# Optimization experiments

Hardware: AMD Instinct MI355X
Metric: run time of the kernel (lower is better)

The kernel has to match this reference:

```python
import jax, jax.numpy as jnp
import numpy as np

N_LAYERS = 4
EPS = 1e-5  # eqx.nn.LayerNorm default


def _kernels(lam, P, B, C, step, L):
    # Annotated-S4 DPLR generating-function kernel (Q = P), vectorized over H channels.
    # lam, P, B, C: (H, N) complex64; step: (H, 1) real. Returns K: (H, L) real.
    omega = jnp.exp((-2j * jnp.pi) * (jnp.arange(L) / L))            # (L,) roots of unity
    g = (2.0 / step) * ((1.0 - omega) / (1.0 + omega))[None, :]      # (H, L) bilinear warp
    c = 2.0 / (1.0 + omega)                                          # (L,)

    def cauchy(v):  # v: (H, N) -> (H, L): sum_n v_n / (g - lambda_n)
        return jnp.sum(v[:, None, :] / (g[:, :, None] - lam[:, None, :]), axis=-1)

    k00 = cauchy(jnp.conj(C) * B)
    k01 = cauchy(jnp.conj(C) * P)
    k10 = cauchy(jnp.conj(P) * B)
    k11 = cauchy(jnp.conj(P) * P)
    at_roots = c[None, :] * (k00 - k01 * (1.0 / (1.0 + k11)) * k10)  # woodbury correction
    return jnp.fft.ifft(at_roots, n=L, axis=-1).real                 # (H, L)


def _causal_conv(u, K):
    # u: (B, L, H) real input, K: (H, L) real kernel -> causal conv along L via zero-padded FFT.
    L = u.shape[1]
    Ud = jnp.fft.rfft(u, n=2 * L, axis=1)                 # (B, F, H)
    Kd = jnp.fft.rfft(K, n=2 * L, axis=-1)                # (H, F)
    return jnp.fft.irfft(Ud * Kd.T[None], n=2 * L, axis=1)[:, :L]


def _forward(x, enc_w, enc_b, dec_w, dec_b, lam_re, lam_im, p_re, p_im, b_re, b_im,
             c_re, c_im, d, log_step, norm_w, norm_b, w1, b1, w2, b2):
    L = x.shape[1]
    h = x @ enc_w.T + enc_b                               # encoder: (B, L, H)
    for i in range(N_LAYERS):
        skip = h
        mu = h.mean(-1, keepdims=True)
        var = ((h - mu) ** 2).mean(-1, keepdims=True)
        hn = (h - mu) / jnp.sqrt(var + EPS) * norm_w[i] + norm_b[i]
        K = _kernels(lam_re[i] + 1j * lam_im[i], p_re[i] + 1j * p_im[i],
                     b_re[i] + 1j * b_im[i], c_re[i] + 1j * c_im[i],
                     jnp.exp(log_step[i])[:, None], L)
        y = _causal_conv(hn, K) + hn * d[i]               # SSM conv + skip-through D term
        y = jax.nn.gelu(y)
        y = (y @ w1[i].T + b1[i]) * jax.nn.sigmoid(y @ w2[i].T + b2[i])  # gated MLP
        h = skip + y
    return h @ dec_w.T + dec_b                            # decoder: (B, L, out)


def setup_inputs() -> dict:
    key = jax.random.key(0)
    B, L, IN, OUT, H, N, NL = 8, 2048, 64, 64, 128, 64, N_LAYERS
    ks = jax.random.split(key, 12)
    rn = lambda k, s, sc: (jax.random.normal(k, s) * sc).astype(jnp.float32)
    return dict(
        x=rn(ks[0], (B, L, IN), 1.0),
        convolve=1,
        enc_w=rn(ks[1], (H, IN), 1.0 / np.sqrt(IN)), enc_b=jnp.zeros((H,), jnp.float32),
        dec_w=rn(ks[2], (OUT, H), 1.0 / np.sqrt(H)), dec_b=jnp.zeros((OUT,), jnp.float32),
        lam_re=-0.5 * jnp.ones((NL, H, N), jnp.float32),  # HiPPO/S4D-style stable poles
        lam_im=jnp.tile(jnp.float32(np.pi) * jnp.arange(N, dtype=jnp.float32), (NL, H, 1)),
        p_re=rn(ks[3], (NL, H, N), 0.5 / np.sqrt(N)), p_im=rn(ks[4], (NL, H, N), 0.5 / np.sqrt(N)),
        b_re=rn(ks[5], (NL, H, N), 1.0), b_im=rn(ks[6], (NL, H, N), 1.0),
        c_re=rn(ks[7], (NL, H, N), 1.0 / np.sqrt(N)), c_im=rn(ks[8], (NL, H, N), 1.0 / np.sqrt(N)),
        d=jnp.ones((NL, H), jnp.float32),
        log_step=(jax.random.uniform(ks[9], (NL, H)) * (np.log(0.1) - np.log(0.001))
                  + np.log(0.001)).astype(jnp.float32),
        norm_w=jnp.ones((NL, H), jnp.float32), norm_b=jnp.zeros((NL, H), jnp.float32),
        w1=rn(ks[10], (NL, H, H), 1.0 / np.sqrt(H)), b1=jnp.zeros((NL, H), jnp.float32),
        w2=rn(ks[11], (NL, H, H), 1.0 / np.sqrt(H)), b2=jnp.zeros((NL, H), jnp.float32),
    )


def reference(x, convolve, enc_w, enc_b, dec_w, dec_b, lam_re, lam_im, p_re, p_im,
              b_re, b_im, c_re, c_im, d, log_step, norm_w, norm_b, w1, b1, w2, b2):
    # convolve is static 1 (True): the FFT-convolution path of the S4 Model.
    return _forward(x, enc_w, enc_b, dec_w, dec_b, lam_re, lam_im, p_re, p_im, b_re, b_im,
                    c_re, c_im, d, log_step, norm_w, norm_b, w1, b1, w2, b2)
```

## Files before the change

kernel.cpp:

```cpp
#include <hip/hip_runtime.h>
#include <hip/hip_bf16.h>


#define Bsz 8
#define Lseq 2048
#define Hdim 128
#define Npol 64
#define NLAYERS 4

typedef __bf16 bf16x8 __attribute__((ext_vector_type(8)));
typedef float f32x16 __attribute__((ext_vector_type(16)));

__device__ __forceinline__ float fast_rcp(float x) { return __builtin_amdgcn_rcpf(x); }
__device__ __forceinline__ float fast_rsq(float x) { return __builtin_amdgcn_rsqf(x); }

__device__ __forceinline__ float2 cmulf(float2 a, float2 b) {
    return make_float2(a.x * b.x - a.y * b.y, a.x * b.y + a.y * b.x);
}
__device__ __forceinline__ float2 cmulc(float2 a, float2 b) {
    return make_float2(a.x * b.x + a.y * b.y, a.y * b.x - a.x * b.y);
}

__device__ __forceinline__ float gelu_f(float v) {
    float z = 0.7978845608028654f * (v + 0.044715f * v * v * v);
    float e = __expf(2.0f * z);
    return v - v * fast_rcp(e + 1.0f);
}

__device__ __forceinline__ int sw(int i) { return (i & ~15) | ((i ^ (i >> 4)) & 15); }

static __device__ const float W16R[8] = {1.f, 0.9238795325f, 0.7071067812f, 0.3826834324f,
                                         0.f, -0.3826834324f, -0.7071067812f, -0.9238795325f};
static __device__ const float W16I[8] = {0.f, -0.3826834324f, -0.7071067812f, -0.9238795325f,
                                         -1.f, -0.9238795325f, -0.7071067812f, -0.3826834324f};
static __device__ const int BR4[16] = {0, 8, 4, 12, 2, 10, 6, 14, 1, 9, 5, 13, 3, 11, 7, 15};
static __device__ const int BR3[8] = {0, 4, 2, 6, 1, 5, 3, 7};

__device__ __forceinline__ float2 twget(const float2* __restrict__ tw, int e) {
    float2 w = tw[e & 2047];
    if (e & 2048) { w.x = -w.x; w.y = -w.y; }
    return w;
}

template <bool INV>
__device__ __forceinline__ void fft16_dif(float2 v[16]) {
#pragma unroll
    for (int mi = 0; mi < 4; mi++) {
        const int m = 8 >> mi;
#pragma unroll
        for (int g = 0; g < 16; g += 2 * m) {
#pragma unroll
            for (int j = 0; j < m; j++) {
                float wr = W16R[j << mi];
                float wi = INV ? -W16I[j << mi] : W16I[j << mi];
                float2 a = v[g + j], b = v[g + j + m];
                float dx = a.x - b.x, dy = a.y - b.y;
                v[g + j] = make_float2(a.x + b.x, a.y + b.y);
                v[g + j + m] = make_float2(dx * wr - dy * wi, dx * wi + dy * wr);
            }
        }
    }
}

template <bool INV>
__device__ __forceinline__ void fft16_dit(float2 v[16]) {
#pragma unroll
    for (int mi = 3; mi >= 0; mi--) {
        const int m = 8 >> mi;
#pragma unroll
        for (int g = 0; g < 16; g += 2 * m) {
#pragma unroll
            for (int j = 0; j < m; j++) {
                float wr = W16R[j << mi];
                float wi = INV ? -W16I[j << mi] : W16I[j << mi];
                float2 a = v[g + j], b = v[g + j + m];
                float bx = b.x * wr - b.y * wi, by = b.x * wi + b.y * wr;
                v[g + j] = make_float2(a.x + bx, a.y + by);
                v[g + j + m] = make_float2(a.x - bx, a.y - by);
            }
        }
    }
}

template <bool INV>
__device__ __forceinline__ void fft8_dif(float2 v[8]) {
#pragma unroll
    for (int mi = 0; mi < 3; mi++) {
        const int m = 4 >> mi;
#pragma unroll
        for (int g = 0; g < 8; g += 2 * m) {
#pragma unroll
            for (int j = 0; j < m; j++) {
                float wr = W16R[j << (mi + 1)];
                float wi = INV ? -W16I[j << (mi + 1)] : W16I[j << (mi + 1)];
                float2 a = v[g + j], b = v[g + j + m];
                float dx = a.x - b.x, dy = a.y - b.y;
                v[g + j] = make_float2(a.x + b.x, a.y + b.y);
                v[g + j + m] = make_float2(dx * wr - dy * wi, dx * wi + dy * wr);
            }
        }
    }
}

__device__ __forceinline__ void fft4096_passA_hz(float2* data, const float2* __restrict__ tw,
                                                 int t, const float2 vin[8]) {
    float2 v[16];
#pragma unroll
    for (int j = 0; j < 8; j++) v[j] = vin[j];
#pragma unroll
    for (int j = 0; j < 8; j++)
        v[j + 8] = cmulf(v[j], make_float2(W16R[j], W16I[j]));
#pragma unroll
    for (int mi = 1; mi < 4; mi++) {
        const int m = 8 >> mi;
#pragma unroll
        for (int g = 0; g < 16; g += 2 * m) {
#pragma unroll
            for (int j = 0; j < m; j++) {
                float wr = W16R[j << mi], wi = W16I[j << mi];
                float2 a = v[g + j], b = v[g + j + m];
                float dx = a.x - b.x, dy = a.y - b.y;
                v[g + j] = make_float2(a.x + b.x, a.y + b.y);
                v[g + j + m] = make_float2(dx * wr - dy * wi, dx * wi + dy * wr);
            }
        }
    }
#pragma unroll
    for (int i = 1; i < 16; i++) v[i] = cmulf(v[i], twget(tw, t * BR4[i]));
#pragma unroll
    for (int i = 0; i < 16; i++) data[sw(i * 256 + t)] = v[i];
}

__device__ __forceinline__ void fft4096_fwd_BC(float2* data, const float2* __restrict__ tw, int t) {
    __syncthreads();
    {
        int j0 = t & 15;
        int base = (t >> 4) * 256 + j0;
        float2 v[16];
#pragma unroll
        for (int k = 0; k < 16; k++) v[k] = data[sw(base + 16 * k)];
        fft16_dif<false>(v);
#pragma unroll
        for (int i = 1; i < 16; i++) v[i] = cmulf(v[i], twget(tw, 16 * j0 * BR4[i]));
#pragma unroll
        for (int i = 0; i < 16; i++) data[sw(base + 16 * i)] = v[i];
    }
    __syncthreads();
    {
        float2 v[16];
#pragma unroll
        for (int k = 0; k < 16; k++) v[k] = data[sw(t * 16 + k)];
        fft16_dif<false>(v);
#pragma unroll
        for (int i = 0; i < 16; i++) data[sw(t * 16 + i)] = v[i];
    }
    __syncthreads();
}

__device__ __forceinline__ void kfft_core(int hh, int t, float* smem,
                                          float2* __restrict__ KdL,
                                          const float2* __restrict__ tw,
                                          const float* __restrict__ lam_re,
                                          const float* __restrict__ lam_im,
                                          const float* __restrict__ p_re,
                                          const float* __restrict__ p_im,
                                          const float* __restrict__ b_re,
                                          const float* __restrict__ b_im,
                                          const float* __restrict__ c_re,
                                          const float* __restrict__ c_im,
                                          const float* __restrict__ log_step) {
    float2* data = (float2*)smem;
    float* ktmp = smem + 8192;
    float4* polA = (float4*)(smem + 10240);
    float4* polB = (float4*)(smem + 10496);
    float* n11S = smem + 10752;
    int baseP = hh * Npol;
    if (t < Npol) {
        int n = t;
        float lr = lam_re[baseP + n], li = lam_im[baseP + n];
        float pr = p_re[baseP + n], pi = p_im[baseP + n];
        float br = b_re[baseP + n], bi = b_im[baseP + n];
        float cr = c_re[baseP + n], ci = c_im[baseP + n];
        polA[n] = make_float4(lr, li, cr * br + ci * bi, cr * bi - ci * br);
        polB[n] = make_float4(cr * pr + ci * pi, cr * pi - ci * pr,
                              pr * br + pi * bi, pr * bi - pi * br);
        n11S[n] = pr * pr + pi * pi;
    }
    __syncthreads();
    {
        float step = expf(log_step[hh]);
        float gs = 2.0f / step;
        float wrv[8], wiv[8];
        float gr[8], gi[8];
#pragma unroll
        for (int j = 0; j < 8; j++) {
            int l = t + 256 * j;
            float ang = -6.283185307179586f * (float)l / (float)Lseq;
            float wr = cosf(ang), wi = sinf(ang);
            wrv[j] = wr; wiv[j] = wi;
            float dr = 1.0f + wr, di = wi;
            float invd2 = fast_rcp(dr * dr + di * di);
            float nr = 1.0f - wr, ni = -wi;
            gr[j] = gs * (nr * dr + ni * di) * invd2;
            gi[j] = gs * (ni * dr - nr * di) * invd2;
        }
        float k00x[8], k00y[8], k01x[8], k01y[8];
        float k10x[8], k10y[8], k11x[8], k11y[8];
#pragma unroll
        for (int j = 0; j < 8; j++) {
            k00x[j] = 0.f; k00y[j] = 0.f; k01x[j] = 0.f; k01y[j] = 0.f;
            k10x[j] = 0.f; k10y[j] = 0.f; k11x[j] = 0.f; k11y[j] = 0.f;
        }
        for (int n = 0; n < Npol; n++) {
            float4 A = polA[n];
            float4 B = polB[n];
            float n11 = n11S[n];
#pragma unroll
            for (int j = 0; j < 8; j++) {
                float er = gr[j] - A.x, ei = gi[j] - A.y;
                float inv2 = fast_rcp(fmaf(er, er, ei * ei));
                float ir = er * inv2;
                float mi = ei * inv2;
                k00x[j] = fmaf(A.z, ir, fmaf(A.w, mi, k00x[j]));
                k00y[j] = fmaf(A.w, ir, fmaf(-A.z, mi, k00y[j]));
                k01x[j] = fmaf(B.x, ir, fmaf(B.y, mi, k01x[j]));
                k01y[j] = fmaf(B.y, ir, fmaf(-B.x, mi, k01y[j]));
                k10x[j] = fmaf(B.z, ir, fmaf(B.w, mi, k10x[j]));
                k10y[j] = fmaf(B.w, ir, fmaf(-B.z, mi, k10y[j]));
                k11x[j] = fmaf(n11, ir, k11x[j]);
                k11y[j] = fmaf(-n11, mi, k11y[j]);
            }
        }
#pragma unroll
        for (int j = 0; j < 8; j++) {
            int l = t + 256 * j;
            float dr = 1.0f + wrv[j], di = wiv[j];
            float invd2 = fast_rcp(dr * dr + di * di);
            float cr2 = 2.0f * dr * invd2, ci2 = -2.0f * di * invd2;
            float wr2 = 1.0f + k11x[j], wi2 = k11y[j];
            float w2inv = fast_rcp(fmaf(wr2, wr2, wi2 * wi2));
            float vr = wr2 * w2inv, vi = -wi2 * w2inv;
            float t1x = k01x[j] * k10x[j] - k01y[j] * k10y[j];
            float t1y = k01x[j] * k10y[j] + k01y[j] * k10x[j];
            float t2x = t1x * vr - t1y * vi, t2y = t1x * vi + t1y * vr;
            float ex = k00x[j] - t2x, ey = k00y[j] - t2y;
            data[sw(l)] = make_float2(cr2 * ex - ci2 * ey, cr2 * ey + ci2 * ex);
        }
    }
    __syncthreads();
    if (t < 128) {
        float2 v[16];
#pragma unroll
        for (int k = 0; k < 16; k++) v[k] = data[sw(t + 128 * k)];
        fft16_dif<true>(v);
#pragma unroll
        for (int i = 1; i < 16; i++) v[i] = cmulc(v[i], twget(tw, 2 * t * BR4[i]));
#pragma unroll
        for (int i = 0; i < 16; i++) data[sw(i * 128 + t)] = v[i];
    }
    __syncthreads();
    if (t < 128) {
        int i2 = t >> 3, j0 = t & 7;
        int base2 = i2 * 128 + j0;
        float2 v[16];
#pragma unroll
        for (int k = 0; k < 16; k++) v[k] = data[sw(base2 + 8 * k)];
        fft16_dif<true>(v);
#pragma unroll
        for (int i = 1; i < 16; i++) v[i] = cmulc(v[i], twget(tw, 32 * j0 * BR4[i]));
#pragma unroll
        for (int i = 0; i < 16; i++) data[sw(base2 + 8 * i)] = v[i];
    }
    __syncthreads();
    {
        float2 v8[8];
#pragma unroll
        for (int k = 0; k < 8; k++) v8[k] = data[sw(t * 8 + k)];
        fft8_dif<true>(v8);
        int r = BR4[t >> 4], s = BR4[t & 15];
#pragma unroll
        for (int i = 0; i < 8; i++) {
            int l = r + 16 * s + 256 * BR3[i];
            ktmp[l] = v8[i].x * (1.0f / 2048.0f);
        }
    }
    __syncthreads();
    {
        float2 vin[8];
#pragma unroll
        for (int k = 0; k < 8; k++) vin[k] = make_float2(ktmp[t + 256 * k], 0.f);
        fft4096_passA_hz(data, tw, t, vin);
    }
    fft4096_fwd_BC(data, tw, t);
    float2* dst = KdL + (size_t)hh * 4096;
#pragma unroll
    for (int k = 0; k < 16; k++) {
        int p = t + 256 * k;
        dst[p] = data[sw(p)];
    }
}

__global__ __launch_bounds__(256, 4) void prep_kernel(const float* __restrict__ w1,
                                                      const float* __restrict__ w2,
                                                      const float* __restrict__ dec_w,
                                                      const float* __restrict__ enc_w,
                                                      float2* __restrict__ tw,
                                                      __bf16* __restrict__ wbf,
                                                      __bf16* __restrict__ decbf,
                                                      __bf16* __restrict__ encbf) {
    int bid = blockIdx.x, t = threadIdx.x;
    if (bid < 8) {
        int k = bid * 256 + t;
        if (k < 2048) {
            double a = -6.283185307179586476925286766559 * (double)k / 4096.0;
            tw[k] = make_float2((float)cos(a), (float)sin(a));
        }
        return;
    }
    if (bid < 264) {
        int i = (bid - 8) * 256 + t;
        int layer = i >> 14, rem = i & 16383;
        wbf[((size_t)layer * 2) * 16384 + rem] = (__bf16)w1[i];
        wbf[((size_t)layer * 2 + 1) * 16384 + rem] = (__bf16)w2[i];
        return;
    }
    if (bid < 296) {
        int i = (bid - 264) * 256 + t;
        decbf[i] = (__bf16)dec_w[i];
        return;
    }
    int i = (bid - 296) * 256 + t;
    encbf[i] = (__bf16)enc_w[i];
}

__global__ __launch_bounds__(256) void kfft_enc_kernel(float2* __restrict__ Kd1,
                                                       const float2* __restrict__ tw,
                                                       const float* __restrict__ x,
                                                       const __bf16* __restrict__ encbf,
                                                       const float* __restrict__ enc_b,
                                                       const float* __restrict__ nw,
                                                       const float* __restrict__ nb,
                                                       float* __restrict__ h,
                                                       float* __restrict__ hnT,
                                                       const float* __restrict__ lam_re,
                                                       const float* __restrict__ lam_im,
                                                       const float* __restrict__ p_re,
                                                       const float* __restrict__ p_im,
                                                       const float* __restrict__ b_re,
                                                       const float* __restrict__ b_im,
                                                       const float* __restrict__ c_re,
                                                       const float* __restrict__ c_im,
                                                       const float* __restrict__ log_step) {
    __shared__ __align__(16) float smem[10816];
    int bid = blockIdx.x, t = threadIdx.x;
    if (bid < 512) {
        int hh = bid & 127, layer = bid >> 7;
        int PN = Hdim * Npol;
        kfft_core(hh, t, smem, Kd1 + (size_t)layer * Hdim * 4096, tw,
                  lam_re + layer * PN, lam_im + layer * PN,
                  p_re + layer * PN, p_im + layer * PN,
                  b_re + layer * PN, b_im + layer * PN,
                  c_re + layer * PN, c_im + layer * PN,
                  log_step + layer * Hdim);
    } else {
        int r0 = (bid - 512) * 32;
        __bf16* ybf = (__bf16*)smem;
        float* dots = smem + 1152;
        float2* mv = (float2*)(smem + 5376);
        int bb = r0 >> 11, l0 = r0 & 2047;
        for (int i = t; i < 32 * 64; i += 256) {
            int r = i >> 6, k = i & 63;
            ybf[r * 72 + k] = (__bf16)x[(size_t)(r0 + r) * 64 + k];
        }
        __syncthreads();
        int wave = t >> 6, lane = t & 63;
        int m = lane & 31, half = lane >> 5;
        bf16x8 a[4];
#pragma unroll
        for (int kk = 0; kk < 4; kk++)
            a[kk] = *(const bf16x8*)&ybf[m * 72 + kk * 16 + half * 8];
        int o = 32 * wave + m;
        const __bf16* wr = encbf + (size_t)o * 64 + half * 8;
        f32x16 acc;
#pragma unroll
        for (int i = 0; i < 16; i++) acc[i] = 0.f;
#pragma unroll
        for (int kk = 0; kk < 4; kk++) {
            bf16x8 bw = *(const bf16x8*)(wr + kk * 16);
            acc = __builtin_amdgcn_mfma_f32_32x32x16_bf16(a[kk], bw, acc, 0, 0, 0);
        }
        float bo = enc_b[o];
#pragma unroll
        for (int reg = 0; reg < 16; reg++) {
            int row = (reg & 3) + 8 * (reg >> 2) + 4 * half;
            dots[row * 132 + o] = acc[reg] + bo;
        }
        __syncthreads();
        {
            int row = t >> 3, lane8 = t & 7;
            float s1 = 0.f, s2 = 0.f;
            int base = row * 132 + lane8 * 16;
#pragma unroll
            for (int q = 0; q < 4; q++) {
                float4 v4 = *(const float4*)&dots[base + 4 * q];
                s1 += v4.x + v4.y + v4.z + v4.w;
                s2 += v4.x * v4.x + v4.y * v4.y + v4.z * v4.z + v4.w * v4.w;
            }
#pragma unroll
            for (int mm = 1; mm < 8; mm <<= 1) { s1 += __shfl_xor(s1, mm); s2 += __shfl_xor(s2, mm); }
            if (lane8 == 0) {
                float mu = s1 * (1.0f / 128.0f);
                float var = s2 * (1.0f / 128.0f) - mu * mu;
                mv[row] = make_float2(mu, fast_rsq(var + 1e-5f));
            }
        }
        __syncthreads();
        {
            int o2 = t & 127, rh = t >> 7;
            float nwc = nw[o2], nbc = nb[o2];
            float hnv[16];
#pragma unroll
            for (int j = 0; j < 16; j++) {
                int r = rh * 16 + j;
                float hvv = dots[r * 132 + o2];
                h[(size_t)(r0 + r) * Hdim + o2] = hvv;
                float2 mvv = mv[r];
                hnv[j] = (hvv - mvv.x) * mvv.y * nwc + nbc;
            }
            float* dst = hnT + ((size_t)bb * Hdim + o2) * Lseq + l0 + rh * 16;
            *(float4*)(dst)      = make_float4(hnv[0],  hnv[1],  hnv[2],  hnv[3]);
            *(float4*)(dst + 4)  = make_float4(hnv[4],  hnv[5],  hnv[6],  hnv[7]);
            *(float4*)(dst + 8)  = make_float4(hnv[8],  hnv[9],  hnv[10], hnv[11]);
            *(float4*)(dst + 12) = make_float4(hnv[12], hnv[13], hnv[14], hnv[15]);
        }
    }
}

__global__ __launch_bounds__(256) void conv_kernel(float* __restrict__ hnT,
                                                   const float2* __restrict__ Kd1,
                                                   const float* __restrict__ dvec,
                                                   const float2* __restrict__ tw) {
    int h = blockIdx.x, bp = blockIdx.y, t = threadIdx.x;
    __shared__ float2 data[4096];
    float* u0 = hnT + ((size_t)(2 * bp) * Hdim + h) * Lseq;
    float* u1 = hnT + ((size_t)(2 * bp + 1) * Hdim + h) * Lseq;
    float2 ureg[8];
    float2 Kreg[16];
    float2 twB[15];
    const int j0 = t & 15;
    const float4* Kp4 = (const float4*)(Kd1 + (size_t)h * 4096 + t * 16);
    {
        float2 vin[8];
#pragma unroll
        for (int k = 0; k < 8; k++) {
            int l = t + 256 * k;
            float2 u2 = make_float2(u0[l], u1[l]);
            ureg[k] = u2;
            vin[k] = u2;
        }
#pragma unroll
        for (int k = 0; k < 8; k++) {
            float4 q = Kp4[k];
            Kreg[2 * k]     = make_float2(q.x, q.y);
            Kreg[2 * k + 1] = make_float2(q.z, q.w);
        }
#pragma unroll
        for (int i = 1; i < 16; i++) twB[i - 1] = twget(tw, 16 * j0 * BR4[i]);
        fft4096_passA_hz(data, tw, t, vin);
    }
    __syncthreads();
    {
        int base = (t >> 4) * 256 + j0;
        float2 v[16];
#pragma unroll
        for (int k = 0; k < 16; k++) v[k] = data[sw(base + 16 * k)];
        fft16_dif<false>(v);
#pragma unroll
        for (int i = 1; i < 16; i++) v[i] = cmulf(v[i], twB[i - 1]);
#pragma unroll
        for (int i = 0; i < 16; i++) data[sw(base + 16 * i)] = v[i];
    }
    __syncthreads();
    {
        const float scale = 1.0f / 4096.0f;
        float2 v[16];
#pragma unroll
        for (int k = 0; k < 16; k++) v[k] = data[sw(t * 16 + k)];
        fft16_dif<false>(v);
#pragma unroll
        for (int i = 0; i < 16; i++) {
            float2 W = cmulf(v[i], Kreg[i]);
            v[i] = make_float2(W.x * scale, W.y * scale);
        }
        fft16_dit<true>(v);
#pragma unroll
        for (int i = 0; i < 16; i++) data[sw(t * 16 + i)] = v[i];
    }
    __syncthreads();
    {
        int base2 = (t >> 4) * 256 + j0;
        float2 v[16];
        v[0] = data[sw(base2)];
#pragma unroll
        for (int i = 1; i < 16; i++)
            v[i] = cmulc(data[sw(base2 + 16 * i)], twB[i - 1]);
        fft16_dit<true>(v);
#pragma unroll
        for (int i = 0; i < 16; i++) data[sw(base2 + 16 * i)] = v[i];
    }
    __syncthreads();
    {
        float2 v[16];
        v[0] = data[sw(t)];
#pragma unroll
        for (int i = 1; i < 16; i++)
            v[i] = cmulc(data[sw(i * 256 + t)], twget(tw, t * BR4[i]));
#pragma unroll
        for (int mi = 3; mi >= 1; mi--) {
            const int m = 8 >> mi;
#pragma unroll
            for (int g = 0; g < 16; g += 2 * m) {
#pragma unroll
                for (int j = 0; j < m; j++) {
                    float wr = W16R[j << mi], wi = -W16I[j << mi];
                    float2 a = v[g + j], bb2 = v[g + j + m];
                    float bx = bb2.x * wr - bb2.y * wi, by = bb2.x * wi + bb2.y * wr;
                    v[g + j] = make_float2(a.x + bx, a.y + by);
                    v[g + j + m] = make_float2(a.x - bx, a.y - by);
                }
            }
        }
#pragma unroll
        for (int j = 0; j < 8; j++) {
            float wr = W16R[j], wi = -W16I[j];
            float2 bb2 = v[j + 8];
            float bx = bb2.x * wr - bb2.y * wi, by = bb2.x * wi + bb2.y * wr;
            v[j] = make_float2(v[j].x + bx, v[j].y + by);
        }
        float dcoef = dvec[h];
#pragma unroll
        for (int k = 0; k < 8; k++) {
            int l = t + 256 * k;
            u0[l] = gelu_f(v[k].x + ureg[k].x * dcoef);
            u1[l] = gelu_f(v[k].y + ureg[k].y * dcoef);
        }
    }
}

__global__ __launch_bounds__(256) void mlp_kernel(const float* __restrict__ yT,
                                                  float* __restrict__ h,
                                                  float* __restrict__ hnT,
                                                  const __bf16* __restrict__ w1b,
                                                  const __bf16* __restrict__ w2b,
                                                  const float* __restrict__ b1,
                                                  const float* __restrict__ b2,
                                                  const float* __restrict__ nw,
                                                  const float* __restrict__ nb) {
    int r0 = blockIdx.x * 32;
    int t = threadIdx.x;
    int wave = t >> 6, lane = t & 63;
    __shared__ __align__(16) __bf16 ybf[32 * 136];
    __shared__ float dots[32 * 132];
    __shared__ float2 mv[32];
    int bb = r0 >> 11, l0 = r0 & 2047;
    for (int i = t; i < 32 * 128; i += 256) {
        int r = i & 31, k = i >> 5;
        ybf[r * 136 + k] = (__bf16)yT[((size_t)bb * Hdim + k) * Lseq + l0 + r];
    }
    __syncthreads();
    int m = lane & 31, half = lane >> 5;
    bf16x8 a[8];
#pragma unroll
    for (int kk = 0; kk < 8; kk++)
        a[kk] = *(const bf16x8*)&ybf[m * 136 + kk * 16 + half * 8];
    int out = 32 * wave + m;
    const __bf16* w1r = w1b + (size_t)out * 128 + half * 8;
    const __bf16* w2r = w2b + (size_t)out * 128 + half * 8;
    f32x16 acc1, acc2;
#pragma unroll
    for (int i = 0; i < 16; i++) { acc1[i] = 0.f; acc2[i] = 0.f; }
#pragma unroll
    for (int kk = 0; kk < 8; kk++) {
        bf16x8 bw1 = *(const bf16x8*)(w1r + kk * 16);
        bf16x8 bw2 = *(const bf16x8*)(w2r + kk * 16);
        acc1 = __builtin_amdgcn_mfma_f32_32x32x16_bf16(a[kk], bw1, acc1, 0, 0, 0);
        acc2 = __builtin_amdgcn_mfma_f32_32x32x16_bf16(a[kk], bw2, acc2, 0, 0, 0);
    }
    float bias1 = b1[out], bias2 = b2[out];
#pragma unroll
    for (int reg = 0; reg < 16; reg++) {
        int row = (reg & 3) + 8 * (reg >> 2) + 4 * half;
        float v1 = acc1[reg] + bias1;
        float v2 = acc2[reg] + bias2;
        float g = fast_rcp(1.0f + __expf(-v2));
        float hv = h[(size_t)(r0 + row) * Hdim + out] + v1 * g;
        dots[row * 132 + out] = hv;
    }
    __syncthreads();
    {
        int row = t >> 3, lane8 = t & 7;
        float s1 = 0.f, s2 = 0.f;
        int base = row * 132 + lane8 * 16;
#pragma unroll
        for (int q = 0; q < 4; q++) {
            float4 v4 = *(const float4*)&dots[base + 4 * q];
            s1 += v4.x + v4.y + v4.z + v4.w;
            s2 += v4.x * v4.x + v4.y * v4.y + v4.z * v4.z + v4.w * v4.w;
        }
#pragma unroll
        for (int mm = 1; mm < 8; mm <<= 1) { s1 += __shfl_xor(s1, mm); s2 += __shfl_xor(s2, mm); }
        if (lane8 == 0) {
            float mu = s1 * (1.0f / 128.0f);
            float var = s2 * (1.0f / 128.0f) - mu * mu;
            mv[row] = make_float2(mu, fast_rsq(var + 1e-5f));
        }
    }
    __syncthreads();
    {
        int o = t & 127, rh = t >> 7;
        float nwc = nw[o], nbc = nb[o];
        float hnv[16];
#pragma unroll
        for (int j = 0; j < 16; j++) {
            int r = rh * 16 + j;
            float hvv = dots[r * 132 + o];
            h[(size_t)(r0 + r) * Hdim + o] = hvv;
            float2 mvv = mv[r];
            hnv[j] = (hvv - mvv.x) * mvv.y * nwc + nbc;
        }
        float* dst = hnT + ((size_t)bb * Hdim + o) * Lseq + l0 + rh * 16;
        *(float4*)(dst)      = make_float4(hnv[0],  hnv[1],  hnv[2],  hnv[3]);
        *(float4*)(dst + 4)  = make_float4(hnv[4],  hnv[5],  hnv[6],  hnv[7]);
        *(float4*)(dst + 8)  = make_float4(hnv[8],  hnv[9],  hnv[10], hnv[11]);
        *(float4*)(dst + 12) = make_float4(hnv[12], hnv[13], hnv[14], hnv[15]);
    }
}

__global__ __launch_bounds__(256) void mlpdec_kernel(const float* __restrict__ yT,
                                                     const float* __restrict__ h,
                                                     const __bf16* __restrict__ w1b,
                                                     const __bf16* __restrict__ w2b,
                                                     const float* __restrict__ b1,
                                                     const float* __restrict__ b2,
                                                     const __bf16* __restrict__ decb,
                                                     const float* __restrict__ dec_bias,
                                                     float* __restrict__ out) {
    int r0 = blockIdx.x * 32;
    int t = threadIdx.x;
    int wave = t >> 6, lane = t & 63;
    __shared__ __align__(16) __bf16 ybf[32 * 136];
    __shared__ float dots[32 * 132];
    int bb = r0 >> 11, l0 = r0 & 2047;
    for (int i = t; i < 32 * 128; i += 256) {
        int r = i & 31, k = i >> 5;
        ybf[r * 136 + k] = (__bf16)yT[((size_t)bb * Hdim + k) * Lseq + l0 + r];
    }
    __syncthreads();
    int m = lane & 31, half = lane >> 5;
    bf16x8 a[8];
#pragma unroll
    for (int kk = 0; kk < 8; kk++)
        a[kk] = *(const bf16x8*)&ybf[m * 136 + kk * 16 + half * 8];
    int outc = 32 * wave + m;
    const __bf16* w1r = w1b + (size_t)outc * 128 + half * 8;
    const __bf16* w2r = w2b + (size_t)outc * 128 + half * 8;
    f32x16 acc1, acc2;
#pragma unroll
    for (int i = 0; i < 16; i++) { acc1[i] = 0.f; acc2[i] = 0.f; }
#pragma unroll
    for (int kk = 0; kk < 8; kk++) {
        bf16x8 bw1 = *(const bf16x8*)(w1r + kk * 16);
        bf16x8 bw2 = *(const bf16x8*)(w2r + kk * 16);
        acc1 = __builtin_amdgcn_mfma_f32_32x32x16_bf16(a[kk], bw1, acc1, 0, 0, 0);
        acc2 = __builtin_amdgcn_mfma_f32_32x32x16_bf16(a[kk], bw2, acc2, 0, 0, 0);
    }
    float bias1 = b1[outc], bias2 = b2[outc];
#pragma unroll
    for (int reg = 0; reg < 16; reg++) {
        int row = (reg & 3) + 8 * (reg >> 2) + 4 * half;
        float v1 = acc1[reg] + bias1;
        float v2 = acc2[reg] + bias2;
        float g = fast_rcp(1.0f + __expf(-v2));
        float hv = h[(size_t)(r0 + row) * Hdim + outc] + v1 * g;
        dots[row * 132 + outc] = hv;
    }
    __syncthreads();
    for (int i = t; i < 32 * 128; i += 256) {
        int r = i >> 7, k = i & 127;
        ybf[r * 136 + k] = (__bf16)dots[r * 132 + k];
    }
    __syncthreads();
    if (wave < 2) {
        bf16x8 a2[8];
#pragma unroll
        for (int kk = 0; kk < 8; kk++)
            a2[kk] = *(const bf16x8*)&ybf[m * 136 + kk * 16 + half * 8];
        int oc = 32 * wave + m;
        const __bf16* wr = decb + (size_t)oc * 128 + half * 8;
        f32x16 acc;
#pragma unroll
        for (int i = 0; i < 16; i++) acc[i] = 0.f;
#pragma unroll
        for (int kk = 0; kk < 8; kk++) {
            bf16x8 bw = *(const bf16x8*)(wr + kk * 16);
            acc = __builtin_amdgcn_mfma_f32_32x32x16_bf16(a2[kk], bw, acc, 0, 0, 0);
        }
        float bo = dec_bias[oc];
#pragma unroll
        for (int reg = 0; reg < 16; reg++) {
            int row = (reg & 3) + 8 * (reg >> 2) + 4 * half;
            out[(size_t)(r0 + row) * 64 + oc] = acc[reg] + bo;
        }
    }
}

extern "C" void kernel_launch(void* const* d_in, const int* in_sizes, int n_in,
                              void* d_out, int out_size, void* d_ws, size_t ws_size,
                              hipStream_t stream) {
    const float* x      = (const float*)d_in[0];
    const float* enc_w  = (const float*)d_in[2];
    const float* enc_b  = (const float*)d_in[3];
    const float* dec_w  = (const float*)d_in[4];
    const float* dec_b  = (const float*)d_in[5];
    const float* lam_re = (const float*)d_in[6];
    const float* lam_im = (const float*)d_in[7];
    const float* p_re   = (const float*)d_in[8];
    const float* p_im   = (const float*)d_in[9];
    const float* b_re   = (const float*)d_in[10];
    const float* b_im   = (const float*)d_in[11];
    const float* c_re   = (const float*)d_in[12];
    const float* c_im   = (const float*)d_in[13];
    const float* dvec   = (const float*)d_in[14];
    const float* lstep  = (const float*)d_in[15];
    const float* norm_w = (const float*)d_in[16];
    const float* norm_b = (const float*)d_in[17];
    const float* w1     = (const float*)d_in[18];
    const float* b1     = (const float*)d_in[19];
    const float* w2     = (const float*)d_in[20];
    const float* b2     = (const float*)d_in[21];
    float* out = (float*)d_out;

    char* ws = (char*)d_ws;
    float2* tw  = (float2*)ws;  ws += 2048 * sizeof(float2);
    float*  h   = (float*)ws;   ws += (size_t)Bsz * Lseq * Hdim * sizeof(float);
    float*  hnT = (float*)ws;   ws += (size_t)Bsz * Lseq * Hdim * sizeof(float);
    float2* Kd1 = (float2*)ws;  ws += (size_t)NLAYERS * Hdim * 4096 * sizeof(float2);
    __bf16* wbf = (__bf16*)ws;  ws += (size_t)NLAYERS * 2 * Hdim * Hdim * sizeof(__bf16);
    __bf16* dbf = (__bf16*)ws;  ws += (size_t)64 * Hdim * sizeof(__bf16);
    __bf16* ebf = (__bf16*)ws;  ws += (size_t)Hdim * 64 * sizeof(__bf16);

    const int nrows = Bsz * Lseq;

    prep_kernel<<<328, 256, 0, stream>>>(w1, w2, dec_w, enc_w, tw, wbf, dbf, ebf);
    kfft_enc_kernel<<<512 + nrows / 32, 256, 0, stream>>>(
        Kd1, tw, x, ebf, enc_b, norm_w, norm_b, h, hnT,
        lam_re, lam_im, p_re, p_im, b_re, b_im, c_re, c_im, lstep);
    for (int L = 0; L < NLAYERS; L++) {
        conv_kernel<<<dim3(Hdim, Bsz / 2), 256, 0, stream>>>(
            hnT, Kd1 + (size_t)L * Hdim * 4096, dvec + L * Hdim, tw);
        const __bf16* w1bL = wbf + (size_t)L * 2 * Hdim * Hdim;
        const __bf16* w2bL = w1bL + Hdim * Hdim;
        if (L < NLAYERS - 1) {
            const float* nwn = norm_w + (L + 1) * Hdim;
            const float* nbn = norm_b + (L + 1) * Hdim;
            mlp_kernel<<<nrows / 32, 256, 0, stream>>>(hnT, h, hnT, w1bL, w2bL,
                                                       b1 + L * Hdim, b2 + L * Hdim,
                                                       nwn, nbn);
        } else {
            mlpdec_kernel<<<nrows / 32, 256, 0, stream>>>(hnT, h, w1bL, w2bL,
                                                          b1 + L * Hdim, b2 + L * Hdim,
                                                          dbf, dec_b, out);
        }
    }
}
```

Baseline: 279.5 us.

## Rewrite conv FFT as radix-8 four-pass with 512 threads and padded LDS

Replaces the radix-16 three-pass 4096-point FFT in the convolution kernel with a radix-8 four-pass (8^4) decomposition, run by 512 threads per block with an 8-element padding scheme in shared memory. The kernel FFT output is permuted (digit reversal) so its frequency order matches the new radix-8 layout used in the pointwise multiply. This roughly halves per-thread register state and doubles threads per block to raise occupancy and latency hiding. In exchange it adds extra LDS passes and barriers, and uses a larger shared buffer.

New measurement: 294.2 us. 1.05x slower.

```diff
diff --git a/kernel.cpp b/kernel.cpp
--- a/kernel.cpp
+++ b/kernel.cpp
@@ -20,6 +20,12 @@
 __device__ __forceinline__ float2 cmulc(float2 a, float2 b) {
     return make_float2(a.x * b.x + a.y * b.y, a.y * b.x - a.x * b.y);
 }
+__device__ __forceinline__ float2 cadd(float2 a, float2 b) {
+    return make_float2(a.x + b.x, a.y + b.y);
+}
+__device__ __forceinline__ float2 csub(float2 a, float2 b) {
+    return make_float2(a.x - b.x, a.y - b.y);
+}
 
 __device__ __forceinline__ float gelu_f(float v) {
     float z = 0.7978845608028654f * (v + 0.044715f * v * v * v);
@@ -28,6 +34,10 @@
 }
 
 __device__ __forceinline__ int sw(int i) { return (i & ~15) | ((i ^ (i >> 4)) & 15); }
+__device__ __forceinline__ int ap(int i) { return i + (i >> 3); }
+__device__ __forceinline__ int dr8(int p) {
+    return ((p & 7) << 9) | (((p >> 3) & 7) << 6) | (((p >> 6) & 7) << 3) | (p >> 9);
+}
 
 static __device__ const float W16R[8] = {1.f, 0.9238795325f, 0.7071067812f, 0.3826834324f,
                                          0.f, -0.3826834324f, -0.7071067812f, -0.9238795325f};
@@ -40,6 +50,52 @@
     float2 w = tw[e & 2047];
     if (e & 2048) { w.x = -w.x; w.y = -w.y; }
     return w;
+}
+
+#define RC8 0.70710678118654752f
+template <bool INV>
+__device__ __forceinline__ float2 rotI(float2 z) {
+    return INV ? make_float2(-z.y, z.x) : make_float2(z.y, -z.x);
+}
+template <bool INV>
+__device__ __forceinline__ float2 rotW(float2 z) {
+    return INV ? make_float2(RC8 * (z.x - z.y), RC8 * (z.x + z.y))
+               : make_float2(RC8 * (z.x + z.y), RC8 * (z.y - z.x));
+}
+template <bool INV>
+__device__ __forceinline__ float2 rotW3(float2 z) {
+    return INV ? make_float2(-RC8 * (z.x + z.y), RC8 * (z.x - z.y))
+               : make_float2(RC8 * (z.y - z.x), -RC8 * (z.x + z.y));
+}
+
+template <bool INV>
+__device__ __forceinline__ void bfly8(float2 v[8]) {
+    float2 a0 = cadd(v[0], v[4]), a1 = cadd(v[1], v[5]);
+    float2 a2 = cadd(v[2], v[6]), a3 = cadd(v[3], v[7]);
+    float2 b0 = csub(v[0], v[4]), b1 = csub(v[1], v[5]);
+    float2 b2 = csub(v[2], v[6]), b3 = csub(v[3], v[7]);
+    float2 c1 = rotW<INV>(b1), c2 = rotI<INV>(b2), c3 = rotW3<INV>(b3);
+    float2 e0 = cadd(a0, a2), e1 = csub(a0, a2);
+    float2 e2 = cadd(a1, a3), e3 = rotI<INV>(csub(a1, a3));
+    v[0] = cadd(e0, e2); v[4] = csub(e0, e2);
+    v[2] = cadd(e1, e3); v[6] = csub(e1, e3);
+    float2 o0 = cadd(b0, c2), o1 = csub(b0, c2);
+    float2 o2 = cadd(c1, c3), o3 = rotI<INV>(csub(c1, c3));
+    v[1] = cadd(o0, o2); v[5] = csub(o0, o2);
+    v[3] = cadd(o1, o3); v[7] = csub(o1, o3);
+}
+
+__device__ __forceinline__ void bfly8_hz(float2 v[8]) {
+    float2 x0 = v[0], x1 = v[1], x2 = v[2], x3 = v[3];
+    float2 c1 = rotW<false>(x1), c2 = rotI<false>(x2), c3 = rotW3<false>(x3);
+    float2 e0 = cadd(x0, x2), e1 = csub(x0, x2);
+    float2 e2 = cadd(x1, x3), e3 = rotI<false>(csub(x1, x3));
+    v[0] = cadd(e0, e2); v[4] = csub(e0, e2);
+    v[2] = cadd(e1, e3); v[6] = csub(e1, e3);
+    float2 o0 = cadd(x0, c2), o1 = csub(x0, c2);
+    float2 o2 = cadd(c1, c3), o3 = rotI<false>(csub(c1, c3));
+    v[1] = cadd(o0, o2); v[5] = csub(o0, o2);
+    v[3] = cadd(o1, o3); v[7] = csub(o1, o3);
 }
 
 template <bool INV>
@@ -57,26 +113,6 @@
                 float dx = a.x - b.x, dy = a.y - b.y;
                 v[g + j] = make_float2(a.x + b.x, a.y + b.y);
                 v[g + j + m] = make_float2(dx * wr - dy * wi, dx * wi + dy * wr);
-            }
-        }
-    }
-}
-
-template <bool INV>
-__device__ __forceinline__ void fft16_dit(float2 v[16]) {
-#pragma unroll
-    for (int mi = 3; mi >= 0; mi--) {
-        const int m = 8 >> mi;
-#pragma unroll
-        for (int g = 0; g < 16; g += 2 * m) {
-#pragma unroll
-            for (int j = 0; j < m; j++) {
-                float wr = W16R[j << mi];
-                float wi = INV ? -W16I[j << mi] : W16I[j << mi];
-                float2 a = v[g + j], b = v[g + j + m];
-                float bx = b.x * wr - b.y * wi, by = b.x * wi + b.y * wr;
-                v[g + j] = make_float2(a.x + bx, a.y + by);
-                v[g + j + m] = make_float2(a.x - bx, a.y - by);
             }
         }
     }
@@ -296,7 +332,9 @@
 #pragma unroll
     for (int k = 0; k < 16; k++) {
         int p = t + 256 * k;
-        dst[p] = data[sw(p)];
+        int kf = dr8(p);
+        int q = 256 * BR4[kf & 15] + 16 * BR4[(kf >> 4) & 15] + BR4[kf >> 8];
+        dst[p] = data[sw(q)];
     }
 }
 
@@ -436,111 +474,119 @@
     }
 }
 
-__global__ __launch_bounds__(256) void conv_kernel(float* __restrict__ hnT,
-                                                   const float2* __restrict__ Kd1,
-                                                   const float* __restrict__ dvec,
-                                                   const float2* __restrict__ tw) {
+__global__ __launch_bounds__(512, 4) void conv_kernel(float* __restrict__ hnT,
+                                                      const float2* __restrict__ Kd1,
+                                                      const float* __restrict__ dvec,
+                                                      const float2* __restrict__ tw) {
     int h = blockIdx.x, bp = blockIdx.y, t = threadIdx.x;
-    __shared__ float2 data[4096];
+    __shared__ float2 data[4608];
     float* u0 = hnT + ((size_t)(2 * bp) * Hdim + h) * Lseq;
     float* u1 = hnT + ((size_t)(2 * bp + 1) * Hdim + h) * Lseq;
-    float2 ureg[8];
-    float2 Kreg[16];
-    float2 twB[15];
-    const int j0 = t & 15;
-    const float4* Kp4 = (const float4*)(Kd1 + (size_t)h * 4096 + t * 16);
-    {
-        float2 vin[8];
-#pragma unroll
-        for (int k = 0; k < 8; k++) {
-            int l = t + 256 * k;
+    float2 ureg[4];
+    float2 Kreg[8];
+    const float4* Kp4 = (const float4*)(Kd1 + (size_t)h * 4096 + t * 8);
+    {
+        float2 v[8];
+#pragma unroll
+        for (int k = 0; k < 4; k++) {
+            int l = t + 512 * k;
             float2 u2 = make_float2(u0[l], u1[l]);
             ureg[k] = u2;
-            vin[k] = u2;
-        }
-#pragma unroll
-        for (int k = 0; k < 8; k++) {
+            v[k] = u2;
+        }
+#pragma unroll
+        for (int k = 0; k < 4; k++) {
             float4 q = Kp4[k];
             Kreg[2 * k]     = make_float2(q.x, q.y);
             Kreg[2 * k + 1] = make_float2(q.z, q.w);
         }
-#pragma unroll
-        for (int i = 1; i < 16; i++) twB[i - 1] = twget(tw, 16 * j0 * BR4[i]);
-        fft4096_passA_hz(data, tw, t, vin);
-    }
-    __syncthreads();
-    {
-        int base = (t >> 4) * 256 + j0;
-        float2 v[16];
-#pragma unroll
-        for (int k = 0; k < 16; k++) v[k] = data[sw(base + 16 * k)];
-        fft16_dif<false>(v);
-#pragma unroll
-        for (int i = 1; i < 16; i++) v[i] = cmulf(v[i], twB[i - 1]);
-#pragma unroll
-        for (int i = 0; i < 16; i++) data[sw(base + 16 * i)] = v[i];
+        bfly8_hz(v);
+#pragma unroll
+        for (int r = 1; r < 8; r++) v[r] = cmulf(v[r], twget(tw, t * r));
+#pragma unroll
+        for (int r = 0; r < 8; r++) data[ap(r * 512 + t)] = v[r];
+    }
+    __syncthreads();
+    {
+        int j = t & 63;
+        int base = (t >> 6) * 512 + j;
+        float2 v[8];
+#pragma unroll
+        for (int m = 0; m < 8; m++) v[m] = data[ap(base + 64 * m)];
+        bfly8<false>(v);
+#pragma unroll
+        for (int r = 1; r < 8; r++) v[r] = cmulf(v[r], twget(tw, 8 * j * r));
+#pragma unroll
+        for (int m = 0; m < 8; m++) data[ap(base + 64 * m)] = v[m];
+    }
+    __syncthreads();
+    {
+        int j = t & 7;
+        int base = (t >> 3) * 64 + j;
+        float2 v[8];
+#pragma unroll
+        for (int m = 0; m < 8; m++) v[m] = data[ap(base + 8 * m)];
+        bfly8<false>(v);
+#pragma unroll
+        for (int r = 1; r < 8; r++) v[r] = cmulf(v[r], twget(tw, 64 * j * r));
+#pragma unroll
+        for (int m = 0; m < 8; m++) data[ap(base + 8 * m)] = v[m];
     }
     __syncthreads();
     {
         const float scale = 1.0f / 4096.0f;
-        float2 v[16];
-#pragma unroll
-        for (int k = 0; k < 16; k++) v[k] = data[sw(t * 16 + k)];
-        fft16_dif<false>(v);
-#pragma unroll
-        for (int i = 0; i < 16; i++) {
-            float2 W = cmulf(v[i], Kreg[i]);
-            v[i] = make_float2(W.x * scale, W.y * scale);
-        }
-        fft16_dit<true>(v);
-#pragma unroll
-        for (int i = 0; i < 16; i++) data[sw(t * 16 + i)] = v[i];
-    }
-    __syncthreads();
-    {
-        int base2 = (t >> 4) * 256 + j0;
-        float2 v[16];
-        v[0] = data[sw(base2)];
-#pragma unroll
-        for (int i = 1; i < 16; i++)
-            v[i] = cmulc(data[sw(base2 + 16 * i)], twB[i - 1]);
-        fft16_dit<true>(v);
-#pragma unroll
-        for (int i = 0; i < 16; i++) data[sw(base2 + 16 * i)] = v[i];
-    }
-    __syncthreads();
-    {
-        float2 v[16];
-        v[0] = data[sw(t)];
-#pragma unroll
-        for (int i = 1; i < 16; i++)
-            v[i] = cmulc(data[sw(i * 256 + t)], twget(tw, t * BR4[i]));
-#pragma unroll
-        for (int mi = 3; mi >= 1; mi--) {
-            const int m = 8 >> mi;
-#pragma unroll
-            for (int g = 0; g < 16; g += 2 * m) {
-#pragma unroll
-                for (int j = 0; j < m; j++) {
-                    float wr = W16R[j << mi], wi = -W16I[j << mi];
-                    float2 a = v[g + j], bb2 = v[g + j + m];
-                    float bx = bb2.x * wr - bb2.y * wi, by = bb2.x * wi + bb2.y * wr;
-                    v[g + j] = make_float2(a.x + bx, a.y + by);
-                    v[g + j + m] = make_float2(a.x - bx, a.y - by);
-                }
-            }
-        }
-#pragma unroll
-        for (int j = 0; j < 8; j++) {
-            float wr = W16R[j], wi = -W16I[j];
-            float2 bb2 = v[j + 8];
-            float bx = bb2.x * wr - bb2.y * wi, by = bb2.x * wi + bb2.y * wr;
-            v[j] = make_float2(v[j].x + bx, v[j].y + by);
-        }
+        int base = t * 8;
+        float2 v[8];
+#pragma unroll
+        for (int m = 0; m < 8; m++) v[m] = data[ap(base + m)];
+        bfly8<false>(v);
+#pragma unroll
+        for (int r = 0; r < 8; r++) {
+            float2 W = cmulf(v[r], Kreg[r]);
+            v[r] = make_float2(W.x * scale, W.y * scale);
+        }
+        bfly8<true>(v);
+#pragma unroll
+        for (int m = 0; m < 8; m++) data[ap(base + m)] = v[m];
+    }
+    __syncthreads();
+    {
+        int j = t & 7;
+        int base = (t >> 3) * 64 + j;
+        float2 v[8];
+#pragma unroll
+        for (int m = 0; m < 8; m++) v[m] = data[ap(base + 8 * m)];
+#pragma unroll
+        for (int r = 1; r < 8; r++) v[r] = cmulc(v[r], twget(tw, 64 * j * r));
+        bfly8<true>(v);
+#pragma unroll
+        for (int m = 0; m < 8; m++) data[ap(base + 8 * m)] = v[m];
+    }
+    __syncthreads();
+    {
+        int j = t & 63;
+        int base = (t >> 6) * 512 + j;
+        float2 v[8];
+#pragma unroll
+        for (int m = 0; m < 8; m++) v[m] = data[ap(base + 64 * m)];
+#pragma unroll
+        for (int r = 1; r < 8; r++) v[r] = cmulc(v[r], twget(tw, 8 * j * r));
+        bfly8<true>(v);
+#pragma unroll
+        for (int m = 0; m < 8; m++) data[ap(base + 64 * m)] = v[m];
+    }
+    __syncthreads();
+    {
+        float2 v[8];
+#pragma unroll
+        for (int r = 0; r < 8; r++) v[r] = data[ap(r * 512 + t)];
+#pragma unroll
+        for (int r = 1; r < 8; r++) v[r] = cmulc(v[r], twget(tw, t * r));
+        bfly8<true>(v);
         float dcoef = dvec[h];
 #pragma unroll
-        for (int k = 0; k < 8; k++) {
-            int l = t + 256 * k;
+        for (int k = 0; k < 4; k++) {
+            int l = t + 512 * k;
             u0[l] = gelu_f(v[k].x + ureg[k].x * dcoef);
             u1[l] = gelu_f(v[k].y + ureg[k].y * dcoef);
         }
@@ -756,7 +802,7 @@
         Kd1, tw, x, ebf, enc_b, norm_w, norm_b, h, hnT,
         lam_re, lam_im, p_re, p_im, b_re, b_im, c_re, c_im, lstep);
     for (int L = 0; L < NLAYERS; L++) {
-        conv_kernel<<<dim3(Hdim, Bsz / 2), 256, 0, stream>>>(
+        conv_kernel<<<dim3(Hdim, Bsz / 2), 512, 0, stream>>>(
             hnT, Kd1 + (size_t)L * Hdim * 4096, dvec + L * Hdim, tw);
         const __bf16* w1bL = wbf + (size_t)L * 2 * Hdim * Hdim;
         const __bf16* w2bL = w1bL + Hdim * Hdim;
```
